# Kernel tuning notes

Measured on AMD Instinct MI355X. Metric: run time of the kernel, lower is better.

Reference implementation:

```python
import jax, jax.numpy as jnp
import numpy as np

N_LABELS = 16
LABEL_DIM = 128
BN_EPS = 1e-5


def setup_inputs() -> dict:
    key = jax.random.key(0)
    k1, k2 = jax.random.split(key, 2)
    B, T, D = 8, 512, 768
    return {
        "features": jax.random.normal(k1, (B, T, D), dtype=jnp.float32),
        "mask": jnp.ones((B, T), dtype=bool),
        "bn_gamma": jnp.ones((D,), dtype=jnp.float32),
        "bn_beta": jnp.zeros((D,), dtype=jnp.float32),
        "ff_w": jax.random.normal(k2, (LABEL_DIM * N_LABELS * 2, D), dtype=jnp.float32) * 0.02,
        "ff_b": jnp.zeros((LABEL_DIM * N_LABELS * 2,), dtype=jnp.float32),
        "label_bias": jnp.zeros((N_LABELS,), dtype=jnp.float32),
    }


def reference(features, mask, bn_gamma, bn_beta, ff_w, ff_b, label_bias):
    B, T, D = features.shape
    m = mask.astype(features.dtype)[..., None]  # [B,T,1]
    denom = jnp.maximum(m.sum(), 1.0)
    # FlatBatchNorm (training mode): stats over masked tokens, zeros elsewhere
    mean = (features * m).sum(axis=(0, 1)) / denom
    var = (((features - mean) ** 2) * m).sum(axis=(0, 1)) / denom
    normed = (features - mean) * jax.lax.rsqrt(var + BN_EPS) * bn_gamma + bn_beta
    feats = normed * m  # res[mask]=flat, zeros elsewhere
    # FFN + relu -> [B,T,n_labels,label_dim,2]
    h = jax.nn.relu(jnp.einsum('btd,od->bto', feats, ff_w) + ff_b)
    h = h.reshape(B, T, N_LABELS, LABEL_DIM, 2)
    start_f = h[..., 0]  # [B,T,L,D]
    end_f = h[..., 1]
    # biaffine span scores: [B, L, T_start, T_end]
    scores = jnp.einsum('bsld,beld->blse', start_f, end_f) + label_bias[None, :, None, None]
    triu = jnp.triu(jnp.ones((T, T), dtype=bool))
    spans_mask = triu[None, None] & mask[:, None, :, None] & mask[:, None, None, :]  # [B,L,T,T] via broadcast
    spans_mask = jnp.broadcast_to(spans_mask, scores.shape)
    return scores, spans_mask
```

## Files before the change

### kernel.cpp

```cpp
#include <hip/hip_runtime.h>

#define B_    8
#define T_    512
#define D_    768
#define L_    16
#define DL_   128
#define NO_   4096
#define M_    4096
#define BN_EPS 1e-5f

typedef __attribute__((ext_vector_type(8))) short short8;
typedef __attribute__((ext_vector_type(4))) float f32x4;

__device__ inline unsigned short f2bf(float x) {
    unsigned int u = __float_as_uint(x);
    unsigned int r = (u + 0x7fffu + ((u >> 16) & 1u)) >> 16;
    return (unsigned short)r;
}

__device__ __forceinline__ void gload_lds16(const unsigned short* g, unsigned short* l) {
    __builtin_amdgcn_global_load_lds(
        (const __attribute__((address_space(1))) unsigned int*)g,
        (__attribute__((address_space(3))) unsigned int*)l, 16, 0, 0);
}

__global__ void k_stats(const float* __restrict__ f, const int* __restrict__ mask,
                        float* __restrict__ stats) {
    int tid = threadIdx.x;
    int t0  = blockIdx.x * 16;
    float s0 = 0.f, s1 = 0.f, s2 = 0.f, q0 = 0.f, q1 = 0.f, q2 = 0.f;
    for (int tt = 0; tt < 16; ++tt) {
        int t = t0 + tt;
        float m = mask[t] ? 1.f : 0.f;
        const float* row = f + (size_t)t * D_;
        float x0 = row[tid];
        float x1 = row[tid + 256];
        float x2 = row[tid + 512];
        s0 += x0 * m; q0 += x0 * x0 * m;
        s1 += x1 * m; q1 += x1 * x1 * m;
        s2 += x2 * m; q2 += x2 * x2 * m;
    }
    atomicAdd(&stats[tid      ], s0);
    atomicAdd(&stats[tid + 256], s1);
    atomicAdd(&stats[tid + 512], s2);
    atomicAdd(&stats[768 + tid      ], q0);
    atomicAdd(&stats[768 + tid + 256], q1);
    atomicAdd(&stats[768 + tid + 512], q2);
    if (tid == 0) {
        int c = 0;
        for (int tt = 0; tt < 16; ++tt) c += (mask[t0 + tt] ? 1 : 0);
        atomicAdd(&stats[1536], (float)c);
    }
}

__global__ void k_finalize(const float* __restrict__ gamma, const float* __restrict__ beta,
                           float* __restrict__ stats) {
    int d = threadIdx.x;
    float denom = fmaxf(stats[1536], 1.f);
    float mean  = stats[d] / denom;
    float var   = fmaxf(stats[768 + d] / denom - mean * mean, 0.f);
    float sc    = gamma[d] * rsqrtf(var + BN_EPS);
    stats[2048 + d] = sc;
    stats[2816 + d] = beta[d] - mean * sc;
}

__global__ void k_normcast(const float4* __restrict__ f4, const float4* __restrict__ w4,
                           const int* __restrict__ mask, const float* __restrict__ stats,
                           unsigned short* __restrict__ featp, unsigned short* __restrict__ wp) {
    int i = blockIdx.x * 256 + threadIdx.x;
    if (i < M_ * D_ / 4) {
        int d4 = i % (D_ / 4);
        int t  = i / (D_ / 4);
        float m = mask[t] ? 1.f : 0.f;
        float4 v = f4[i];
        int d = d4 * 4;
        float r0 = (v.x * stats[2048 + d + 0] + stats[2816 + d + 0]) * m;
        float r1 = (v.y * stats[2048 + d + 1] + stats[2816 + d + 1]) * m;
        float r2 = (v.z * stats[2048 + d + 2] + stats[2816 + d + 2]) * m;
        float r3 = (v.w * stats[2048 + d + 3] + stats[2816 + d + 3]) * m;
        ushort4 o;
        o.x = f2bf(r0); o.y = f2bf(r1); o.z = f2bf(r2); o.w = f2bf(r3);
        ((ushort4*)featp)[i] = o;
    } else {
        int j = i - M_ * D_ / 4;
        float4 v = w4[j];
        ushort4 o;
        o.x = f2bf(v.x); o.y = f2bf(v.y); o.z = f2bf(v.z); o.w = f2bf(v.w);
        ((ushort4*)wp)[j] = o;
    }
}

__launch_bounds__(256)
__global__ void k_ffn(const unsigned short* __restrict__ A, const unsigned short* __restrict__ W,
                      const float* __restrict__ bias,
                      unsigned short* __restrict__ startp, unsigned short* __restrict__ endp) {
    __shared__ alignas(16) unsigned short As[128 * 32];
    __shared__ alignas(16) unsigned short Bs[128 * 32];
    int tid  = threadIdx.x;
    int bm   = blockIdx.x, bn = blockIdx.y;
    int wave = tid >> 6, lane = tid & 63;
    int wm = wave >> 1, wn = wave & 1;
    int lr = lane & 15, quad = lane >> 4;
    f32x4 acc[4][4] = {};
    const int K = D_;
    int srow   = (lane >> 2);
    int scolsh = (lane & 3) * 8;
    for (int k0 = 0; k0 < K; k0 += 32) {
#pragma unroll
        for (int p = 0; p < 2; ++p) {
            int c   = wave * 2 + p;
            int row = c * 16 + srow;
            gload_lds16(A + (size_t)(bm * 128 + row) * K + k0 + scolsh, &As[c * 512]);
            gload_lds16(W + (size_t)(bn * 128 + row) * K + k0 + scolsh, &Bs[c * 512]);
        }
        __syncthreads();
        short8 a[4], b[4];
#pragma unroll
        for (int i = 0; i < 4; ++i) a[i] = *(const short8*)&As[(wm * 64 + i * 16 + lr) * 32 + quad * 8];
#pragma unroll
        for (int i = 0; i < 4; ++i) b[i] = *(const short8*)&Bs[(wn * 64 + i * 16 + lr) * 32 + quad * 8];
#pragma unroll
        for (int i = 0; i < 4; ++i)
#pragma unroll
            for (int j = 0; j < 4; ++j)
                acc[i][j] = __builtin_amdgcn_mfma_f32_16x16x32_bf16(a[i], b[j], acc[i][j], 0, 0, 0);
        __syncthreads();
    }
#pragma unroll
    for (int i = 0; i < 4; ++i) {
#pragma unroll
        for (int j = 0; j < 4; ++j) {
            int col  = bn * 128 + wn * 64 + j * 16 + lr;
            int l    = col >> 8;
            int dd   = (col >> 1) & 127;
            int cbit = col & 1;
            unsigned short* dst = cbit ? endp : startp;
            float bv = bias[col];
#pragma unroll
            for (int r = 0; r < 4; ++r) {
                int row = bm * 128 + wm * 64 + i * 16 + quad * 4 + r;
                float v = acc[i][j][r] + bv;
                v = fmaxf(v, 0.f);
                int bb = row >> 9, tt = row & 511;
                dst[(((size_t)(bb * 16 + l) * 512 + tt) << 7) + dd] = f2bf(v);
            }
        }
    }
}

__launch_bounds__(256)
__global__ void k_biaffine(const unsigned short* __restrict__ startp,
                           const unsigned short* __restrict__ endp,
                           const int* __restrict__ mask,
                           const float* __restrict__ lbias,
                           float* __restrict__ out_scores, float* __restrict__ out_mask) {
    __shared__ alignas(16) unsigned short As[128 * 64];
    __shared__ alignas(16) unsigned short Bs[128 * 64];
    int tid = threadIdx.x;
    int bm = blockIdx.x, bn = blockIdx.y;
    int bl = blockIdx.z;
    int b  = bl >> 4;
    const unsigned short* A  = startp + (size_t)bl * 512 * 128;
    const unsigned short* Bp = endp   + (size_t)bl * 512 * 128;
    int wave = tid >> 6, lane = tid & 63;
    int wm = wave >> 1, wn = wave & 1;
    int lr = lane & 15, quad = lane >> 4;
    f32x4 acc[4][4] = {};
    int srow = lane >> 3;
    for (int half = 0; half < 2; ++half) {
#pragma unroll
        for (int p = 0; p < 4; ++p) {
            int c   = wave * 4 + p;
            int row = c * 8 + srow;
            int gl  = (lane & 7) ^ (row & 7);
            gload_lds16(A  + (size_t)(bm * 128 + row) * DL_ + half * 64 + gl * 8, &As[c * 512]);
            gload_lds16(Bp + (size_t)(bn * 128 + row) * DL_ + half * 64 + gl * 8, &Bs[c * 512]);
        }
        __syncthreads();
#pragma unroll
        for (int kk = 0; kk < 2; ++kk) {
            short8 a[4], bb[4];
#pragma unroll
            for (int i = 0; i < 4; ++i) {
                int row = wm * 64 + i * 16 + lr;
                int gp  = (kk * 4 + quad) ^ (row & 7);
                a[i] = *(const short8*)&As[row * 64 + gp * 8];
            }
#pragma unroll
            for (int j = 0; j < 4; ++j) {
                int row = wn * 64 + j * 16 + lr;
                int gp  = (kk * 4 + quad) ^ (row & 7);
                bb[j] = *(const short8*)&Bs[row * 64 + gp * 8];
            }
#pragma unroll
            for (int i = 0; i < 4; ++i)
#pragma unroll
                for (int j = 0; j < 4; ++j)
                    acc[i][j] = __builtin_amdgcn_mfma_f32_16x16x32_bf16(a[i], bb[j], acc[i][j], 0, 0, 0);
        }
        __syncthreads();
    }
    float lb = lbias[bl & 15];
    float* obase = out_scores + (size_t)bl * 512 * 512;
    float* mbase = out_mask   + (size_t)bl * 512 * 512;
    float msv[4][4];
#pragma unroll
    for (int i = 0; i < 4; ++i)
#pragma unroll
        for (int r = 0; r < 4; ++r) {
            int s = bm * 128 + wm * 64 + i * 16 + quad * 4 + r;
            msv[i][r] = mask[b * 512 + s] ? 1.f : 0.f;
        }
#pragma unroll
    for (int j = 0; j < 4; ++j) {
        int e = bn * 128 + wn * 64 + j * 16 + lr;
        float me = mask[b * 512 + e] ? 1.f : 0.f;
#pragma unroll
        for (int i = 0; i < 4; ++i) {
#pragma unroll
            for (int r = 0; r < 4; ++r) {
                int s = bm * 128 + wm * 64 + i * 16 + quad * 4 + r;
                size_t off = (size_t)s * 512 + e;
                obase[off] = acc[i][j][r] + lb;
                mbase[off] = (s <= e) ? msv[i][r] * me : 0.f;
            }
        }
    }
}

extern "C" void kernel_launch(void* const* d_in, const int* in_sizes, int n_in,
                              void* d_out, int out_size, void* d_ws, size_t ws_size,
                              hipStream_t stream) {
    const float* features = (const float*)d_in[0];
    const int*   mask     = (const int*)d_in[1];
    const float* gamma    = (const float*)d_in[2];
    const float* beta     = (const float*)d_in[3];
    const float* ffw      = (const float*)d_in[4];
    const float* ffb      = (const float*)d_in[5];
    const float* lbias    = (const float*)d_in[6];

    float* out_scores = (float*)d_out;
    float* out_mask   = out_scores + (size_t)B_ * L_ * T_ * T_;

    char* ws = (char*)d_ws;
    float*          stats  = (float*)ws;
    unsigned short* feats  = (unsigned short*)(ws + 16384);
    unsigned short* wbf    = (unsigned short*)(ws + 16384 + 6291456);
    unsigned short* startp = (unsigned short*)(ws + 12599296);
    unsigned short* endp   = (unsigned short*)(ws + 29376512);

    hipMemsetAsync(ws, 0, 16384, stream);
    k_stats<<<256, 256, 0, stream>>>(features, mask, stats);
    k_finalize<<<1, 768, 0, stream>>>(gamma, beta, stats);
    k_normcast<<<6144, 256, 0, stream>>>((const float4*)features, (const float4*)ffw,
                                         mask, stats, feats, wbf);
    dim3 g1(32, 32);
    k_ffn<<<g1, 256, 0, stream>>>(feats, wbf, ffb, startp, endp);
    dim3 g2(4, 4, 128);
    k_biaffine<<<g2, 256, 0, stream>>>(startp, endp, mask, lbias, out_scores, out_mask);
}
```

Baseline: 408.4 us.

## Pipeline FFN GEMM with 4-stage swizzled LDS ring and nontemporal biaffine stores

Rewrites the FFN GEMM to use 512 threads and 8 waves with a 64-wide K step. A 4-slot LDS ring is prefetched two stages ahead through global_load_lds with vmcnt waits, which replaces the two __syncthreads per iteration. LDS rows use an XOR swizzle to avoid bank conflicts, and s_setprio raises priority around the MFMA bursts. The biaffine output and mask writes become nontemporal stores to reduce cache pollution from the large output. LDS use grows to 128KB per block, which limits occupancy and makes correctness depend on the hand-written wait counts.

```diff
diff --git a/kernel.cpp b/kernel.cpp
--- a/kernel.cpp
+++ b/kernel.cpp
@@ -90,47 +90,94 @@
     }
 }
 
-__launch_bounds__(256)
+__launch_bounds__(512, 2)
 __global__ void k_ffn(const unsigned short* __restrict__ A, const unsigned short* __restrict__ W,
                       const float* __restrict__ bias,
                       unsigned short* __restrict__ startp, unsigned short* __restrict__ endp) {
-    __shared__ alignas(16) unsigned short As[128 * 32];
-    __shared__ alignas(16) unsigned short Bs[128 * 32];
+    __shared__ alignas(16) unsigned short LA[4][8192];
+    __shared__ alignas(16) unsigned short LB[4][8192];
     int tid  = threadIdx.x;
     int bm   = blockIdx.x, bn = blockIdx.y;
     int wave = tid >> 6, lane = tid & 63;
-    int wm = wave >> 1, wn = wave & 1;
+    int wm = wave >> 2, wn = wave & 3;
     int lr = lane & 15, quad = lane >> 4;
-    f32x4 acc[4][4] = {};
-    const int K = D_;
-    int srow   = (lane >> 2);
-    int scolsh = (lane & 3) * 8;
-    for (int k0 = 0; k0 < K; k0 += 32) {
+    int srow = lane >> 3;
+    int sg   = (lane & 7) ^ srow;
+    const unsigned short* asrc[2];
+    const unsigned short* bsrc[2];
+#pragma unroll
+    for (int p = 0; p < 2; ++p) {
+        int c = wave * 2 + p;
+        asrc[p] = A + (size_t)(bm * 128 + c * 8 + srow) * D_ + sg * 8;
+        bsrc[p] = W + (size_t)(bn * 128 + c * 8 + srow) * D_ + sg * 8;
+    }
+    int aoff[4][2], boff[2][2];
+#pragma unroll
+    for (int i = 0; i < 4; ++i)
+#pragma unroll
+        for (int kk = 0; kk < 2; ++kk) {
+            int row = wm * 64 + i * 16 + lr;
+            aoff[i][kk] = row * 64 + ((kk * 4 + quad) ^ (row & 7)) * 8;
+        }
+#pragma unroll
+    for (int j = 0; j < 2; ++j)
+#pragma unroll
+        for (int kk = 0; kk < 2; ++kk) {
+            int row = wn * 32 + j * 16 + lr;
+            boff[j][kk] = row * 64 + ((kk * 4 + quad) ^ (row & 7)) * 8;
+        }
+    f32x4 acc[4][2] = {};
+#pragma unroll
+    for (int t = 0; t < 2; ++t) {
 #pragma unroll
         for (int p = 0; p < 2; ++p) {
-            int c   = wave * 2 + p;
-            int row = c * 16 + srow;
-            gload_lds16(A + (size_t)(bm * 128 + row) * K + k0 + scolsh, &As[c * 512]);
-            gload_lds16(W + (size_t)(bn * 128 + row) * K + k0 + scolsh, &Bs[c * 512]);
-        }
-        __syncthreads();
-        short8 a[4], b[4];
-#pragma unroll
-        for (int i = 0; i < 4; ++i) a[i] = *(const short8*)&As[(wm * 64 + i * 16 + lr) * 32 + quad * 8];
-#pragma unroll
-        for (int i = 0; i < 4; ++i) b[i] = *(const short8*)&Bs[(wn * 64 + i * 16 + lr) * 32 + quad * 8];
+            int c = wave * 2 + p;
+            gload_lds16(asrc[p] + t * 64, &LA[t][c * 512]);
+            gload_lds16(bsrc[p] + t * 64, &LB[t][c * 512]);
+        }
+    }
+#pragma unroll
+    for (int t = 0; t < 12; ++t) {
+        if (t == 11) asm volatile("s_waitcnt vmcnt(0)\ns_barrier" ::: "memory");
+        else         asm volatile("s_waitcnt vmcnt(4)\ns_barrier" ::: "memory");
+        const unsigned short* la = LA[t & 3];
+        const unsigned short* lb = LB[t & 3];
+        short8 af[4][2], bf[2][2];
 #pragma unroll
         for (int i = 0; i < 4; ++i)
 #pragma unroll
-            for (int j = 0; j < 4; ++j)
-                acc[i][j] = __builtin_amdgcn_mfma_f32_16x16x32_bf16(a[i], b[j], acc[i][j], 0, 0, 0);
-        __syncthreads();
+            for (int kk = 0; kk < 2; ++kk)
+                af[i][kk] = *(const short8*)&la[aoff[i][kk]];
+#pragma unroll
+        for (int j = 0; j < 2; ++j)
+#pragma unroll
+            for (int kk = 0; kk < 2; ++kk)
+                bf[j][kk] = *(const short8*)&lb[boff[j][kk]];
+        if (t < 10) {
+            int ss = (t + 2) & 3;
+            int ko = (t + 2) * 64;
+#pragma unroll
+            for (int p = 0; p < 2; ++p) {
+                int c = wave * 2 + p;
+                gload_lds16(asrc[p] + ko, &LA[ss][c * 512]);
+                gload_lds16(bsrc[p] + ko, &LB[ss][c * 512]);
+            }
+        }
+        __builtin_amdgcn_s_setprio(1);
+#pragma unroll
+        for (int kk = 0; kk < 2; ++kk)
+#pragma unroll
+            for (int i = 0; i < 4; ++i)
+#pragma unroll
+                for (int j = 0; j < 2; ++j)
+                    acc[i][j] = __builtin_amdgcn_mfma_f32_16x16x32_bf16(af[i][kk], bf[j][kk], acc[i][j], 0, 0, 0);
+        __builtin_amdgcn_s_setprio(0);
     }
 #pragma unroll
     for (int i = 0; i < 4; ++i) {
 #pragma unroll
-        for (int j = 0; j < 4; ++j) {
-            int col  = bn * 128 + wn * 64 + j * 16 + lr;
+        for (int j = 0; j < 2; ++j) {
+            int col  = bn * 128 + wn * 32 + j * 16 + lr;
             int l    = col >> 8;
             int dd   = (col >> 1) & 127;
             int cbit = col & 1;
@@ -221,8 +268,8 @@
             for (int r = 0; r < 4; ++r) {
                 int s = bm * 128 + wm * 64 + i * 16 + quad * 4 + r;
                 size_t off = (size_t)s * 512 + e;
-                obase[off] = acc[i][j][r] + lb;
-                mbase[off] = (s <= e) ? msv[i][r] * me : 0.f;
+                __builtin_nontemporal_store(acc[i][j][r] + lb, &obase[off]);
+                __builtin_nontemporal_store((s <= e) ? msv[i][r] * me : 0.f, &mbase[off]);
             }
         }
     }
@@ -255,7 +302,7 @@
     k_normcast<<<6144, 256, 0, stream>>>((const float4*)features, (const float4*)ffw,
                                          mask, stats, feats, wbf);
     dim3 g1(32, 32);
-    k_ffn<<<g1, 256, 0, stream>>>(feats, wbf, ffb, startp, endp);
+    k_ffn<<<g1, 512, 0, stream>>>(feats, wbf, ffb, startp, endp);
     dim3 g2(4, 4, 128);
     k_biaffine<<<g2, 256, 0, stream>>>(startp, endp, mask, lbias, out_scores, out_mask);
 }
```

Result: faster. 379.0 us (-7.2%).
